# Optimization experiments

Hardware: AMD Instinct MI355X
Metric: run time of the kernel (lower is better)

The kernel has to match this reference:

```python
import jax, jax.numpy as jnp
import numpy as np

B, S, C, DM, NH, DH = 1, 2048, 2048, 768, 12, 64
LN_EPS = 1e-9


def setup_inputs() -> dict:
    rng = jax.random.key(0)
    ks = jax.random.split(rng, 24)
    f32 = jnp.float32
    p = 0.02  # param init scale
    inp = {
        'query': jax.random.normal(ks[0], (B, S, DM), f32),
        'key': jax.random.normal(ks[1], (B, C, DM), f32),
        'value': jax.random.normal(ks[2], (B, C, DM), f32),
        'phi': jax.random.normal(ks[3], (S, DM), f32) * p,
        'pi': jax.random.normal(ks[4], (S, DM), f32) * p,
        'psi': jax.random.normal(ks[5], (C, DM), f32) * p,
        'omega': jax.random.normal(ks[6], (C, DM), f32) * p,
        'cls_mask': jnp.ones((S, C), f32),
        'token_type_mat': jax.random.randint(ks[7], (B, S, C), 0, 2).astype(bool),
        'attention_mask': jnp.ones((B, C), jnp.int32),
        # learned parameters
        'Wq': jax.random.normal(ks[8], (DM, NH * DH), f32) * p,
        'Wk': jax.random.normal(ks[9], (DM, NH * DH), f32) * p,
        'bk': jnp.zeros((NH * DH,), f32),
        'Wv': jax.random.normal(ks[10], (DM, NH * DH), f32) * p,
        'bv': jnp.zeros((NH * DH,), f32),
        'r_w_bias': jax.random.normal(ks[11], (NH, DH), f32) * p,
        'r_r_bias': jax.random.normal(ks[12], (NH, DH), f32) * p,
        'r_kernel': jax.random.normal(ks[13], (DM, NH, DH), f32) * p,
        'r_s_bias': jax.random.normal(ks[14], (NH, DH), f32) * p,
        'seg_embed': jax.random.normal(ks[15], (2, NH, DH), f32) * p,
        'Wo': jax.random.normal(ks[16], (NH * DH, DM), f32) * p,
        'bo': jnp.zeros((DM,), f32),
        'ln_scale': jnp.ones((DM,), f32),
        'ln_bias': jnp.zeros((DM,), f32),
    }
    return inp


def reference(query, key, value, phi, pi, psi, omega, cls_mask,
              token_type_mat, attention_mask,
              Wq, Wk, bk, Wv, bv, r_w_bias, r_r_bias, r_kernel,
              r_s_bias, seg_embed, Wo, bo, ln_scale, ln_bias):
    b, s, _ = query.shape
    c = key.shape[1]
    scale = 1.0 / DH ** 0.5
    # head projections
    q = (query @ Wq).reshape(b, s, NH, DH) * scale          # [b,i,n,h]
    k = (key @ Wk + bk).reshape(b, c, NH, DH)                # [b,j,n,h]
    v = (value @ Wv + bv).reshape(b, c, NH, DH)
    # content score
    content = jnp.einsum('binh,bjnh->bnij', q + r_w_bias * scale, k)
    # factorized relative positional attention
    qr = jnp.einsum('binh,dnh->bind', q + r_r_bias * scale, r_kernel)  # [b,i,n,d_model]
    pos = (jnp.einsum('bind,jd->bnij', qr * phi[:, None], psi)
           + jnp.einsum('bind,jd->bnij', qr * pi[:, None], omega))
    pos = pos * cls_mask
    # token-type attention
    tt_bias = jnp.einsum('binh,snh->bnis', q + r_s_bias * scale, seg_embed)  # [b,n,i,2]
    diff_tt, same_tt = jnp.split(tt_bias, 2, axis=-1)  # each [b,n,i,1]
    tt = jnp.where(token_type_mat[:, None], same_tt, diff_tt) * cls_mask
    # combine, mask, softmax
    score = content + pos + tt
    score = score - 1000000.0 * (1.0 - attention_mask[:, None, None].astype(jnp.float32))
    prob = jax.nn.softmax(score, axis=-1)  # [b,n,i,j]
    attn_vec = jnp.einsum('bnij,bjnh->binh', prob, v).reshape(b, s, NH * DH)
    attn_out = attn_vec @ Wo + bo
    # residual + layernorm
    x = query + attn_out
    mu = x.mean(-1, keepdims=True)
    var = x.var(-1, keepdims=True)
    return (x - mu) * jax.lax.rsqrt(var + LN_EPS) * ln_scale + ln_bias
```

## Files before the change

kernel.cpp:

```cpp
#include <hip/hip_runtime.h>
#include <hip/hip_bf16.h>
#include <stddef.h>

#define DEVINL __device__ __forceinline__

typedef __attribute__((ext_vector_type(8))) short short8;
typedef __attribute__((ext_vector_type(4))) float f32x4;

static constexpr int S_LEN = 2048;
static constexpr int C_LEN = 2048;
static constexpr int DMODEL = 768;
static constexpr int NHEAD = 12;
static constexpr int DHEAD = 64;
static constexpr float SCALE = 0.125f;

DEVINL float bf2f(short s) {
    union { unsigned u; float f; } v;
    v.u = ((unsigned)(unsigned short)s) << 16;
    return v.f;
}
DEVINL short f2bf(float f) {
    union { float f; unsigned u; } v;
    v.f = f;
    unsigned r = v.u + 0x7FFFu + ((v.u >> 16) & 1u);
    return (short)(r >> 16);
}
DEVINL f32x4 zero4() { f32x4 z; z[0]=0.f; z[1]=0.f; z[2]=0.f; z[3]=0.f; return z; }

DEVINL int swz(int width, int row, int col) {
    return (row * width + col) ^ ((row & 7) << 3);
}

DEVINL void gl_lds16(const short* g, short* l) {
    __builtin_amdgcn_global_load_lds(
        (const __attribute__((address_space(1))) void*)g,
        (__attribute__((address_space(3))) void*)l,
        16, 0, 0);
}

template<int ROWS, int WIDTH>
DEVINL void stage_lds_swz(short* lds_tile, const short* src, int src_stride, int w, int lane) {
    constexpr int CPR = WIDTH / 8;
    constexpr int CH  = ROWS * CPR;
    for (int c0 = w * 64; c0 < CH; c0 += 256) {
        int chunk = c0 + lane;
        int row   = chunk / CPR;
        int ccol  = chunk % CPR;
        int scol  = ccol ^ (row & 7);
        gl_lds16(src + (size_t)row * src_stride + scol * 8, lds_tile + c0 * 8);
    }
}

DEVINL void stage_addcol(short* dst, const short* src, const float* p1, const float* p2,
                         int col0, int src_stride) {
    for (int c = threadIdx.x; c < 1024; c += 256) {
        int row = c >> 3;
        int cc  = (c & 7) * 8;
        short8 a = *(const short8*)(src + (size_t)row * src_stride + cc);
        short8 r;
#pragma unroll
        for (int e = 0; e < 8; ++e)
            r[e] = f2bf(bf2f(a[e]) + (p1[col0 + cc + e] - p2[col0 + cc + e]) * SCALE);
        *(short8*)(dst + swz(64, row, cc)) = r;
    }
}

DEVINL void mfma_step_128(const short* As, const short* Bs, f32x4 acc[4][4],
                          int wr, int wc, int lane) {
#pragma unroll
    for (int kk = 0; kk < 64; kk += 32) {
        short8 a[4], b[4];
#pragma unroll
        for (int mi = 0; mi < 4; ++mi)
            a[mi] = *(const short8*)(As + swz(64, wr*64 + mi*16 + (lane & 15), kk + (lane >> 4) * 8));
#pragma unroll
        for (int ni = 0; ni < 4; ++ni)
            b[ni] = *(const short8*)(Bs + swz(64, wc*64 + ni*16 + (lane & 15), kk + (lane >> 4) * 8));
#pragma unroll
        for (int mi = 0; mi < 4; ++mi)
#pragma unroll
            for (int ni = 0; ni < 4; ++ni)
                acc[mi][ni] = __builtin_amdgcn_mfma_f32_16x16x32_bf16(a[mi], b[ni], acc[mi][ni], 0, 0, 0);
    }
}

DEVINL void mfma_2x2(const short* As, const short* Bs, f32x4 acc[2][4],
                     int wr2, int wc2, int lane) {
#pragma unroll
    for (int kk = 0; kk < 64; kk += 32) {
        short8 a[2], b[4];
#pragma unroll
        for (int mi = 0; mi < 2; ++mi)
            a[mi] = *(const short8*)(As + swz(64, wr2*32 + mi*16 + (lane & 15), kk + (lane >> 4) * 8));
#pragma unroll
        for (int nj = 0; nj < 4; ++nj)
            b[nj] = *(const short8*)(Bs + swz(64, wc2*64 + nj*16 + (lane & 15), kk + (lane >> 4) * 8));
#pragma unroll
        for (int mi = 0; mi < 2; ++mi)
#pragma unroll
            for (int nj = 0; nj < 4; ++nj)
                acc[mi][nj] = __builtin_amdgcn_mfma_f32_16x16x32_bf16(a[mi], b[nj], acc[mi][nj], 0, 0, 0);
    }
}

template<int KSTEPS>
DEVINL void gemm128_body(const short* A, const short* Bt, short* As, short* Bs,
                         f32x4 acc[4][4], int wr, int wc, int lane, int w) {
    for (int ks = 0; ks < KSTEPS; ++ks) {
        if (ks) __syncthreads();
        stage_lds_swz<128, 64>(As, A + ks * 64, DMODEL, w, lane);
        stage_lds_swz<128, 64>(Bs, Bt + ks * 64, DMODEL, w, lane);
        __syncthreads();
        mfma_step_128(As, Bs, acc, wr, wc, lane);
    }
}

__global__ void conv_kernel(const float* q, const float* k, const float* v,
                            const float* psi, const float* omega, const float* rk,
                            const float* cls, const int* ttm,
                            short* qc, short* kc, short* vc,
                            short* psc, short* omc, short* rkc,
                            short* clsb, char* ttm8) {
    int z = blockIdx.z;
    if (z == 7) {
        for (int i = blockIdx.x * 256 + threadIdx.x; i < 1048576; i += gridDim.x * 256) {
            int4 t = *(const int4*)(ttm + (size_t)i * 4);
            char4 o;
            o.x = (char)t.x; o.y = (char)t.y; o.z = (char)t.z; o.w = (char)t.w;
            *(char4*)(ttm8 + (size_t)i * 4) = o;
        }
        return;
    }
    const float* src; short* dst; int n4;
    switch (z) {
        case 0: src = q;     dst = qc;   n4 = 393216;  break;
        case 1: src = k;     dst = kc;   n4 = 393216;  break;
        case 2: src = v;     dst = vc;   n4 = 393216;  break;
        case 3: src = psi;   dst = psc;  n4 = 393216;  break;
        case 4: src = omega; dst = omc;  n4 = 393216;  break;
        case 5: src = rk;    dst = rkc;  n4 = 147456;  break;
        default: src = cls;  dst = clsb; n4 = 1048576; break;
    }
    for (int i = blockIdx.x * 256 + threadIdx.x; i < n4; i += gridDim.x * 256) {
        float4 f = *(const float4*)(src + (size_t)i * 4);
        short4 o;
        o.x = f2bf(f.x); o.y = f2bf(f.y); o.z = f2bf(f.z); o.w = f2bf(f.w);
        *(short4*)(dst + (size_t)i * 4) = o;
    }
}

__global__ void transpose_kernel(const float* wq, const float* wk, const float* wv, const float* wo,
                                 short* wqt, short* wkt, short* wvt, short* wot) {
    __shared__ float tile[64][65];
    int z = blockIdx.z;
    const float* src = (z == 0) ? wq : (z == 1) ? wk : (z == 2) ? wv : wo;
    short*       dst = (z == 0) ? wqt : (z == 1) ? wkt : (z == 2) ? wvt : wot;
    int r0 = blockIdx.x * 64, c0 = blockIdx.y * 64;
    for (int e = threadIdx.x; e < 4096; e += 256) {
        int rr = e >> 6, cc = e & 63;
        tile[rr][cc] = src[(size_t)(r0 + rr) * DMODEL + c0 + cc];
    }
    __syncthreads();
    for (int e = threadIdx.x; e < 4096; e += 256) {
        int rr = e >> 6, cc = e & 63;
        dst[(size_t)(c0 + rr) * DMODEL + r0 + cc] = f2bf(tile[cc][rr]);
    }
}

__global__ __launch_bounds__(256, 2)
void qkv_kernel(const short* qc, const short* kc, const short* vc,
                const short* wqt, const short* wkt, const short* wvt,
                const float* bk, const float* bv, const float* rw,
                short* qw_a, short* kpack, short* vt) {
    __shared__ short As[128 * 64], Bs[128 * 64];
    int z = blockIdx.z;
    const short* A  = (z == 0) ? qc  : (z == 1) ? kc  : vc;
    const short* Bt = (z == 0) ? wqt : (z == 1) ? wkt : wvt;
    int i0 = blockIdx.x * 128, c0 = blockIdx.y * 128;
    int t = threadIdx.x, lane = t & 63, w = t >> 6, wr = w >> 1, wc = w & 1;

    f32x4 acc[4][4];
#pragma unroll
    for (int mi = 0; mi < 4; ++mi)
#pragma unroll
        for (int ni = 0; ni < 4; ++ni) acc[mi][ni] = zero4();

    gemm128_body<12>(A + (size_t)i0 * DMODEL, Bt + (size_t)c0 * DMODEL, As, Bs, acc, wr, wc, lane, w);

#pragma unroll
    for (int mi = 0; mi < 4; ++mi)
#pragma unroll
        for (int ni = 0; ni < 4; ++ni)
#pragma unroll
            for (int r = 0; r < 4; ++r) {
                int row = i0 + wr*64 + mi*16 + ((lane >> 4) << 2) + r;
                int col = c0 + wc*64 + ni*16 + (lane & 15);
                float v = acc[mi][ni][r];
                if (z == 0) {
                    qw_a[(size_t)row * DMODEL + col] = f2bf(v * SCALE + rw[col] * SCALE);
                } else if (z == 1) {
                    float vv = v + bk[col];
                    kpack[((size_t)(col >> 6) * C_LEN + row) * DHEAD + (col & 63)] = f2bf(vv);
                } else {
                    float vv = v + bv[col];
                    vt[((size_t)(col >> 6) * DHEAD + (col & 63)) * C_LEN + row] = f2bf(vv);
                }
            }
}

__global__ __launch_bounds__(256, 2)
void qr_kernel(const short* qwa, const short* rkc, const float* rr, const float* rw,
               const float* phi, const float* pi_, short* a1, short* a2, int n_base) {
    __shared__ short As[128 * 64], Bs[128 * 64];
    int nl = blockIdx.z, n = n_base + nl;
    int i0 = blockIdx.x * 128, d0 = blockIdx.y * 128;
    int t = threadIdx.x, lane = t & 63, w = t >> 6, wr = w >> 1, wc = w & 1;

    f32x4 acc[4][4];
#pragma unroll
    for (int mi = 0; mi < 4; ++mi)
#pragma unroll
        for (int ni = 0; ni < 4; ++ni) acc[mi][ni] = zero4();

    stage_addcol(As, qwa + (size_t)i0 * DMODEL + n * DHEAD, rr, rw, n * DHEAD, DMODEL);
    stage_lds_swz<128, 64>(Bs, rkc + (size_t)d0 * DMODEL + n * DHEAD, DMODEL, w, lane);
    __syncthreads();
    mfma_step_128(As, Bs, acc, wr, wc, lane);

#pragma unroll
    for (int mi = 0; mi < 4; ++mi)
#pragma unroll
        for (int ni = 0; ni < 4; ++ni)
#pragma unroll
            for (int r = 0; r < 4; ++r) {
                int row = i0 + wr*64 + mi*16 + ((lane >> 4) << 2) + r;
                int col = d0 + wc*64 + ni*16 + (lane & 15);
                float v = acc[mi][ni][r];
                size_t src = (size_t)row * DMODEL + col;
                size_t dst = ((size_t)nl * S_LEN + row) * DMODEL + col;
                a1[dst] = f2bf(v * phi[src]);
                a2[dst] = f2bf(v * pi_[src]);
            }
}

__global__ void ttb_kernel(const short* qwa, const float* seg, const float* rs, const float* rw,
                           float* ttd, float* tts) {
    int idx = blockIdx.x * 256 + threadIdx.x;
    int n = idx >> 11, i = idx & 2047;
    const short* q  = qwa + (size_t)i * DMODEL + n * DHEAD;
    const float* e0 = seg + n * DHEAD;
    const float* e1 = seg + NHEAD * DHEAD + n * DHEAD;
    float s0 = 0.f, s1 = 0.f;
#pragma unroll
    for (int h = 0; h < DHEAD; ++h) {
        float qv = bf2f(q[h]) + (rs[n * DHEAD + h] - rw[n * DHEAD + h]) * SCALE;
        s0 += qv * e0[h];
        s1 += qv * e1[h];
    }
    ttd[n * S_LEN + i] = s0;
    tts[n * S_LEN + i] = s1;
}

__global__ __launch_bounds__(256, 3)
void flash_kernel(const short* qw_a, const short* kpack, const short* a1, const short* a2,
                  const short* psc, const short* omc, const short* clsb,
                  const char* ttm8, const int* amask, const float* ttd, const float* tts,
                  const short* vt, short* pacc, float* pm, float* pl, int n_base) {
    __shared__ short dbuf[2 * 12288];
    short* Ps = dbuf;

    int nl = blockIdx.y, n = n_base + nl;
    int i0 = blockIdx.x * 64;
    int jt = blockIdx.z;
    int j0 = jt * 128;

    int t = threadIdx.x, lane = t & 63, w = t >> 6;
    int wr2 = w >> 1, wc2 = w & 1;
    int lrow = lane >> 4;
    int lcol = lane & 15;

    f32x4 acc_c[2][4], acc_p[2][4];
#pragma unroll
    for (int mi = 0; mi < 2; ++mi)
#pragma unroll
        for (int nj = 0; nj < 4; ++nj) { acc_c[mi][nj] = zero4(); acc_p[mi][nj] = zero4(); }

    const short* a_base = a1 + ((size_t)nl * S_LEN + i0) * DMODEL;
    const short* a2base = a2 + ((size_t)nl * S_LEN + i0) * DMODEL;
    const short* p_base = psc + (size_t)j0 * DMODEL;
    const short* o_base = omc + (size_t)j0 * DMODEL;

    auto STAGE = [&](int b, int s) {
        short* B = dbuf + b * 12288;
        if (s == 0) {
            stage_lds_swz<64, 64>(B, qw_a + (size_t)i0 * DMODEL + n * DHEAD, DMODEL, w, lane);
            stage_lds_swz<128, 64>(B + 4096, kpack + ((size_t)n * C_LEN + j0) * DHEAD, DHEAD, w, lane);
        } else {
            int d0 = ((s - 1) % 12) * 64;
            const short* asrc = ((s <= 12) ? a_base : a2base) + d0;
            const short* bsrc = ((s <= 12) ? p_base : o_base) + d0;
            stage_lds_swz<64, 64>(B, asrc, DMODEL, w, lane);
            stage_lds_swz<128, 64>(B + 4096, bsrc, DMODEL, w, lane);
        }
    };

    STAGE(0, 0);
    STAGE(1, 1);

    for (int ks = 0; ks < 25; ++ks) {
        int cur = ks & 1;
        short* B = dbuf + cur * 12288;
        if (ks < 24) { asm volatile("s_waitcnt vmcnt(6)" ::: "memory"); }
        else         { asm volatile("s_waitcnt vmcnt(4)" ::: "memory"); }
        __builtin_amdgcn_sched_barrier(0);
        __builtin_amdgcn_s_barrier();
        if (ks == 0) mfma_2x2(B, B + 4096, acc_c, wr2, wc2, lane);
        else         mfma_2x2(B, B + 4096, acc_p, wr2, wc2, lane);
        asm volatile("s_waitcnt lgkmcnt(0)" ::: "memory");
        __builtin_amdgcn_sched_barrier(0);
        __builtin_amdgcn_s_barrier();
        if (ks < 23)
            STAGE(cur, ks + 2);
        else if (ks == 23)
            stage_lds_swz<64, 128>(dbuf + 12288, vt + (size_t)(n * DHEAD) * C_LEN + j0, C_LEN, w, lane);
    }

    float tdiff[2][4], tsame[2][4];
#pragma unroll
    for (int mi = 0; mi < 2; ++mi)
#pragma unroll
        for (int r = 0; r < 4; ++r) {
            int ig = i0 + wr2*32 + mi*16 + lrow*4 + r;
            tdiff[mi][r] = ttd[n * S_LEN + ig];
            tsame[mi][r] = tts[n * S_LEN + ig];
        }
    float pbuf[2][4][4];
    float m[2][4];
#pragma unroll
    for (int mi = 0; mi < 2; ++mi)
#pragma unroll
        for (int r = 0; r < 4; ++r) m[mi][r] = -1.0e9f;
#pragma unroll
    for (int nj = 0; nj < 4; ++nj) {
        int jg = j0 + wc2*64 + nj*16 + lcol;
        float pen = 1.0e6f * (1.0f - (float)amask[jg]);
#pragma unroll
        for (int mi = 0; mi < 2; ++mi)
#pragma unroll
            for (int r = 0; r < 4; ++r) {
                int ig = i0 + wr2*32 + mi*16 + lrow*4 + r;
                size_t eidx = (size_t)ig * C_LEN + jg;
                float clsv = bf2f(clsb[eidx]);
                float ttv  = ttm8[eidx] ? tsame[mi][r] : tdiff[mi][r];
                float sc = acc_c[mi][nj][r] + clsv * (acc_p[mi][nj][r] + ttv) - pen;
                pbuf[mi][nj][r] = sc;
                m[mi][r] = fmaxf(m[mi][r], sc);
            }
    }
#pragma unroll
    for (int mi = 0; mi < 2; ++mi)
#pragma unroll
        for (int r = 0; r < 4; ++r) {
            float v = m[mi][r];
            v = fmaxf(v, __shfl_xor(v, 1));
            v = fmaxf(v, __shfl_xor(v, 2));
            v = fmaxf(v, __shfl_xor(v, 4));
            v = fmaxf(v, __shfl_xor(v, 8));
            m[mi][r] = v;
        }
    float l[2][4];
#pragma unroll
    for (int mi = 0; mi < 2; ++mi)
#pragma unroll
        for (int r = 0; r < 4; ++r) l[mi][r] = 0.f;
#pragma unroll
    for (int nj = 0; nj < 4; ++nj)
#pragma unroll
        for (int mi = 0; mi < 2; ++mi)
#pragma unroll
            for (int r = 0; r < 4; ++r) {
                float pv = __expf(fminf(pbuf[mi][nj][r] - m[mi][r], 0.0f));
                pbuf[mi][nj][r] = pv;
                l[mi][r] += pv;
            }
#pragma unroll
    for (int mi = 0; mi < 2; ++mi)
#pragma unroll
        for (int r = 0; r < 4; ++r) {
            float v = l[mi][r];
            v += __shfl_xor(v, 1);
            v += __shfl_xor(v, 2);
            v += __shfl_xor(v, 4);
            v += __shfl_xor(v, 8);
            l[mi][r] = v;
        }

#pragma unroll
    for (int mi = 0; mi < 2; ++mi)
#pragma unroll
        for (int nj = 0; nj < 4; ++nj)
#pragma unroll
            for (int r = 0; r < 4; ++r)
                Ps[swz(128, wr2*32 + mi*16 + lrow*4 + r, wc2*64 + nj*16 + lcol)] = f2bf(pbuf[mi][nj][r]);

    __syncthreads();

    f32x4 out_acc[2][4];
#pragma unroll
    for (int mi = 0; mi < 2; ++mi)
#pragma unroll
        for (int nh = 0; nh < 4; ++nh) out_acc[mi][nh] = zero4();
#pragma unroll
    for (int kk = 0; kk < 2; ++kk) {
        short8 pa[2];
#pragma unroll
        for (int mi = 0; mi < 2; ++mi)
            pa[mi] = *(const short8*)(Ps + swz(128, wr2*32 + mi*16 + (lane & 15), wc2*64 + kk*32 + lrow*8));
#pragma unroll
        for (int nh = 0; nh < 4; ++nh) {
            short8 vb = *(const short8*)(dbuf + 12288 + swz(128, nh*16 + (lane & 15), wc2*64 + kk*32 + lrow*8));
#pragma unroll
            for (int mi = 0; mi < 2; ++mi)
                out_acc[mi][nh] = __builtin_amdgcn_mfma_f32_16x16x32_bf16(pa[mi], vb, out_acc[mi][nh], 0, 0, 0);
        }
    }

    int jp = jt * 2 + wc2;
#pragma unroll
    for (int mi = 0; mi < 2; ++mi)
#pragma unroll
        for (int r = 0; r < 4; ++r) {
            int ig = i0 + wr2*32 + mi*16 + lrow*4 + r;
            size_t base = ((size_t)(nl * S_LEN + ig) * 32 + jp);
            if (lcol == 0) { pm[base] = m[mi][r]; pl[base] = l[mi][r]; }
#pragma unroll
            for (int nh = 0; nh < 4; ++nh)
                pacc[base * 64 + nh*16 + lcol] = f2bf(out_acc[mi][nh][r]);
        }
}

__global__ void combine_kernel(const short* pacc, const float* pm, const float* pl,
                               short* avec, int n_base) {
    int idx = blockIdx.x * 256 + threadIdx.x;
    int h8 = idx & 7;
    int rest = idx >> 3;
    int i  = rest & 2047;
    int nl = rest >> 11;
    size_t b = ((size_t)nl * S_LEN + i) * 32;
    float M = -1.0e30f;
#pragma unroll
    for (int p = 0; p < 32; ++p) M = fmaxf(M, pm[b + p]);
    float L = 0.f;
    float o[8] = {0.f,0.f,0.f,0.f,0.f,0.f,0.f,0.f};
#pragma unroll
    for (int p = 0; p < 32; ++p) {
        float wg = __expf(pm[b + p] - M);
        L += wg * pl[b + p];
        short8 v = *(const short8*)(pacc + (b + p) * 64 + h8 * 8);
#pragma unroll
        for (int e = 0; e < 8; ++e) o[e] += wg * bf2f(v[e]);
    }
    float invL = 1.0f / L;
    short8 r;
#pragma unroll
    for (int e = 0; e < 8; ++e) r[e] = f2bf(o[e] * invL);
    *(short8*)(avec + (size_t)i * DMODEL + (n_base + nl) * DHEAD + h8 * 8) = r;
}

__global__ __launch_bounds__(256, 2)
void outproj_kernel(const short* avec, const short* wot, const float* bo,
                    const float* query, float* X) {
    __shared__ short As[128 * 64], Bs[128 * 64];
    int i0 = blockIdx.x * 128, c0 = blockIdx.y * 128;
    int t = threadIdx.x, lane = t & 63, w = t >> 6, wr = w >> 1, wc = w & 1;

    f32x4 acc[4][4];
#pragma unroll
    for (int mi = 0; mi < 4; ++mi)
#pragma unroll
        for (int ni = 0; ni < 4; ++ni) acc[mi][ni] = zero4();

    gemm128_body<12>(avec + (size_t)i0 * DMODEL, wot + (size_t)c0 * DMODEL, As, Bs, acc, wr, wc, lane, w);

#pragma unroll
    for (int mi = 0; mi < 4; ++mi)
#pragma unroll
        for (int ni = 0; ni < 4; ++ni)
#pragma unroll
            for (int r = 0; r < 4; ++r) {
                int row = i0 + wr*64 + mi*16 + ((lane >> 4) << 2) + r;
                int col = c0 + wc*64 + ni*16 + (lane & 15);
                float v = acc[mi][ni][r] + bo[col];
                X[(size_t)row * DMODEL + col] = v + query[(size_t)row * DMODEL + col];
            }
}

__global__ void ln_kernel(const float* X, const float* gam, const float* bet, float* out) {
    int row = blockIdx.x, t = threadIdx.x;
    const float* xr = X + (size_t)row * DMODEL;
    float x0 = xr[t], x1 = xr[t + 256], x2 = xr[t + 512];
    float s = x0 + x1 + x2;
    float q = x0*x0 + x1*x1 + x2*x2;
#pragma unroll
    for (int d = 1; d < 64; d <<= 1) { s += __shfl_xor(s, d); q += __shfl_xor(q, d); }
    __shared__ float rs_[4], rq_[4];
    int w = t >> 6, lane = t & 63;
    if (lane == 0) { rs_[w] = s; rq_[w] = q; }
    __syncthreads();
    s = rs_[0] + rs_[1] + rs_[2] + rs_[3];
    q = rq_[0] + rq_[1] + rq_[2] + rq_[3];
    float mu  = s * (1.0f / 768.0f);
    float var = q * (1.0f / 768.0f) - mu * mu;
    float rstd = rsqrtf(fmaxf(var, 0.0f) + 1e-9f);
    out[(size_t)row * DMODEL + t]       = (x0 - mu) * rstd * gam[t]       + bet[t];
    out[(size_t)row * DMODEL + t + 256] = (x1 - mu) * rstd * gam[t + 256] + bet[t + 256];
    out[(size_t)row * DMODEL + t + 512] = (x2 - mu) * rstd * gam[t + 512] + bet[t + 512];
}

extern "C" void kernel_launch(void* const* d_in, const int* in_sizes, int n_in,
                              void* d_out, int out_size, void* d_ws, size_t ws_size,
                              hipStream_t stream) {
    const float* query = (const float*)d_in[0];
    const float* key   = (const float*)d_in[1];
    const float* value = (const float*)d_in[2];
    const float* phi   = (const float*)d_in[3];
    const float* pi_   = (const float*)d_in[4];
    const float* psi   = (const float*)d_in[5];
    const float* omega = (const float*)d_in[6];
    const float* cls   = (const float*)d_in[7];
    const int*   ttm   = (const int*)d_in[8];
    const int*   am    = (const int*)d_in[9];
    const float* Wq    = (const float*)d_in[10];
    const float* Wk    = (const float*)d_in[11];
    const float* bk    = (const float*)d_in[12];
    const float* Wv    = (const float*)d_in[13];
    const float* bv    = (const float*)d_in[14];
    const float* rw    = (const float*)d_in[15];
    const float* rr    = (const float*)d_in[16];
    const float* rk    = (const float*)d_in[17];
    const float* rs    = (const float*)d_in[18];
    const float* seg   = (const float*)d_in[19];
    const float* Wo    = (const float*)d_in[20];
    const float* bo    = (const float*)d_in[21];
    const float* lng   = (const float*)d_in[22];
    const float* lnb   = (const float*)d_in[23];

    char* ws = (char*)d_ws;
    constexpr size_t SZ_W   = 768ull * 768 * 2;
    constexpr size_t SZ_SD  = 2048ull * 768 * 2;
    constexpr size_t SZ_3H  = 3ull * 2048 * 768 * 2;
    constexpr size_t OFF_WQT = 0;
    constexpr size_t OFF_WKT = OFF_WQT + SZ_W;
    constexpr size_t OFF_WVT = OFF_WKT + SZ_W;
    constexpr size_t OFF_WOT = OFF_WVT + SZ_W;
    constexpr size_t OFF_RKC = OFF_WOT + SZ_W;
    constexpr size_t OFF_QC  = OFF_RKC + SZ_W;
    constexpr size_t OFF_KC  = OFF_QC  + SZ_SD;
    constexpr size_t OFF_VC  = OFF_KC  + SZ_SD;
    constexpr size_t OFF_PSC = OFF_VC  + SZ_SD;
    constexpr size_t OFF_OMC = OFF_PSC + SZ_SD;
    constexpr size_t OFF_QWA = OFF_OMC + SZ_SD;
    constexpr size_t OFF_KP  = OFF_QWA + SZ_SD;
    constexpr size_t OFF_VT  = OFF_KP  + SZ_SD;
    constexpr size_t OFF_A1  = OFF_VT  + SZ_SD;
    constexpr size_t OFF_A2  = OFF_A1  + SZ_3H;
    constexpr size_t OFF_CLB = OFF_A2  + SZ_3H;
    constexpr size_t OFF_TT8 = OFF_CLB + 2048ull * 2048 * 2;
    constexpr size_t OFF_TTD = OFF_TT8 + 2048ull * 2048;
    constexpr size_t OFF_TTS = OFF_TTD + 12ull * 2048 * 4;
    constexpr size_t OFF_AV  = OFF_TTS + 12ull * 2048 * 4;
    constexpr size_t OFF_PA  = OFF_AV  + SZ_SD;
    constexpr size_t OFF_PM  = OFF_PA  + 3ull * 2048 * 32 * 64 * 2;
    constexpr size_t OFF_PL  = OFF_PM  + 3ull * 2048 * 32 * 4;
    constexpr size_t OFF_X   = OFF_PA;
    constexpr size_t NEED    = OFF_PL + 3ull * 2048 * 32 * 4;

    if (ws_size < NEED) return;

    short* wqt  = (short*)(ws + OFF_WQT);
    short* wkt  = (short*)(ws + OFF_WKT);
    short* wvt  = (short*)(ws + OFF_WVT);
    short* wot  = (short*)(ws + OFF_WOT);
    short* rkc  = (short*)(ws + OFF_RKC);
    short* qc   = (short*)(ws + OFF_QC);
    short* kc   = (short*)(ws + OFF_KC);
    short* vc   = (short*)(ws + OFF_VC);
    short* psc  = (short*)(ws + OFF_PSC);
    short* omc  = (short*)(ws + OFF_OMC);
    short* qwa  = (short*)(ws + OFF_QWA);
    short* kp   = (short*)(ws + OFF_KP);
    short* vt   = (short*)(ws + OFF_VT);
    short* a1   = (short*)(ws + OFF_A1);
    short* a2   = (short*)(ws + OFF_A2);
    short* clsb = (short*)(ws + OFF_CLB);
    char*  ttm8 = (char*)(ws + OFF_TT8);
    float* ttd  = (float*)(ws + OFF_TTD);
    float* tts  = (float*)(ws + OFF_TTS);
    short* avec = (short*)(ws + OFF_AV);
    short* pacc = (short*)(ws + OFF_PA);
    float* pm   = (float*)(ws + OFF_PM);
    float* pl   = (float*)(ws + OFF_PL);
    float* X    = (float*)(ws + OFF_X);

    conv_kernel<<<dim3(768, 1, 8), 256, 0, stream>>>(query, key, value, psi, omega, rk, cls, ttm,
                                                     qc, kc, vc, psc, omc, rkc, clsb, ttm8);
    transpose_kernel<<<dim3(12, 12, 4), 256, 0, stream>>>(Wq, Wk, Wv, Wo, wqt, wkt, wvt, wot);
    qkv_kernel<<<dim3(16, 6, 3), 256, 0, stream>>>(qc, kc, vc, wqt, wkt, wvt,
                                                   bk, bv, rw, qwa, kp, vt);
    ttb_kernel<<<96, 256, 0, stream>>>(qwa, seg, rs, rw, ttd, tts);
    for (int nb = 0; nb < NHEAD; nb += 3) {
        qr_kernel<<<dim3(16, 6, 3), 256, 0, stream>>>(qwa, rkc, rr, rw, phi, pi_, a1, a2, nb);
        flash_kernel<<<dim3(32, 3, 16), 256, 0, stream>>>(qwa, kp, a1, a2, psc, omc, clsb,
                                                          ttm8, am, ttd, tts, vt, pacc, pm, pl, nb);
        combine_kernel<<<192, 256, 0, stream>>>(pacc, pm, pl, avec, nb);
    }
    outproj_kernel<<<dim3(16, 6), 256, 0, stream>>>(avec, wot, bo, query, X);
    ln_kernel<<<2048, 256, 0, stream>>>(X, lng, lnb, (float*)d_out);
}
```

Baseline: 461.3 us.

## Split flash tile across eight waves instead of four

The flash kernel now launches 512 threads per block. Each of eight waves computes a 16x64 sub-tile instead of a 32x64 one, which halves the per-wave accumulators and MFMA work. LDS staging loops stride by 512 threads and the vmcnt waits are halved to match the fewer loads per thread. This aims to raise latency hiding and wave-level parallelism within the 64x128 tile. In exchange, A-fragment reuse across mi drops and each wave does more LDS traffic per MFMA.

```diff
diff --git a/kernel.cpp b/kernel.cpp
--- a/kernel.cpp
+++ b/kernel.cpp
@@ -38,11 +38,11 @@
         16, 0, 0);
 }
 
-template<int ROWS, int WIDTH>
+template<int ROWS, int WIDTH, int NT = 256>
 DEVINL void stage_lds_swz(short* lds_tile, const short* src, int src_stride, int w, int lane) {
     constexpr int CPR = WIDTH / 8;
     constexpr int CH  = ROWS * CPR;
-    for (int c0 = w * 64; c0 < CH; c0 += 256) {
+    for (int c0 = w * 64; c0 < CH; c0 += NT) {
         int chunk = c0 + lane;
         int row   = chunk / CPR;
         int ccol  = chunk % CPR;
@@ -84,22 +84,18 @@
     }
 }
 
-DEVINL void mfma_2x2(const short* As, const short* Bs, f32x4 acc[2][4],
-                     int wr2, int wc2, int lane) {
+DEVINL void mfma_8w(const short* As, const short* Bs, f32x4 acc[4],
+                    int wr4, int wc, int lane) {
 #pragma unroll
     for (int kk = 0; kk < 64; kk += 32) {
-        short8 a[2], b[4];
-#pragma unroll
-        for (int mi = 0; mi < 2; ++mi)
-            a[mi] = *(const short8*)(As + swz(64, wr2*32 + mi*16 + (lane & 15), kk + (lane >> 4) * 8));
+        short8 a = *(const short8*)(As + swz(64, wr4*16 + (lane & 15), kk + (lane >> 4) * 8));
+        short8 b[4];
 #pragma unroll
         for (int nj = 0; nj < 4; ++nj)
-            b[nj] = *(const short8*)(Bs + swz(64, wc2*64 + nj*16 + (lane & 15), kk + (lane >> 4) * 8));
-#pragma unroll
-        for (int mi = 0; mi < 2; ++mi)
-#pragma unroll
-            for (int nj = 0; nj < 4; ++nj)
-                acc[mi][nj] = __builtin_amdgcn_mfma_f32_16x16x32_bf16(a[mi], b[nj], acc[mi][nj], 0, 0, 0);
+            b[nj] = *(const short8*)(Bs + swz(64, wc*64 + nj*16 + (lane & 15), kk + (lane >> 4) * 8));
+#pragma unroll
+        for (int nj = 0; nj < 4; ++nj)
+            acc[nj] = __builtin_amdgcn_mfma_f32_16x16x32_bf16(a, b[nj], acc[nj], 0, 0, 0);
     }
 }
 
@@ -261,7 +257,7 @@
     tts[n * S_LEN + i] = s1;
 }
 
-__global__ __launch_bounds__(256, 3)
+__global__ __launch_bounds__(512, 2)
 void flash_kernel(const short* qw_a, const short* kpack, const short* a1, const short* a2,
                   const short* psc, const short* omc, const short* clsb,
                   const char* ttm8, const int* amask, const float* ttd, const float* tts,
@@ -275,15 +271,13 @@
     int j0 = jt * 128;
 
     int t = threadIdx.x, lane = t & 63, w = t >> 6;
-    int wr2 = w >> 1, wc2 = w & 1;
+    int wr4 = w >> 1, wc = w & 1;
     int lrow = lane >> 4;
     int lcol = lane & 15;
 
-    f32x4 acc_c[2][4], acc_p[2][4];
-#pragma unroll
-    for (int mi = 0; mi < 2; ++mi)
-#pragma unroll
-        for (int nj = 0; nj < 4; ++nj) { acc_c[mi][nj] = zero4(); acc_p[mi][nj] = zero4(); }
+    f32x4 acc_c[4], acc_p[4];
+#pragma unroll
+    for (int nj = 0; nj < 4; ++nj) { acc_c[nj] = zero4(); acc_p[nj] = zero4(); }
 
     const short* a_base = a1 + ((size_t)nl * S_LEN + i0) * DMODEL;
     const short* a2base = a2 + ((size_t)nl * S_LEN + i0) * DMODEL;
@@ -293,14 +287,14 @@
     auto STAGE = [&](int b, int s) {
         short* B = dbuf + b * 12288;
         if (s == 0) {
-            stage_lds_swz<64, 64>(B, qw_a + (size_t)i0 * DMODEL + n * DHEAD, DMODEL, w, lane);
-            stage_lds_swz<128, 64>(B + 4096, kpack + ((size_t)n * C_LEN + j0) * DHEAD, DHEAD, w, lane);
+            stage_lds_swz<64, 64, 512>(B, qw_a + (size_t)i0 * DMODEL + n * DHEAD, DMODEL, w, lane);
+            stage_lds_swz<128, 64, 512>(B + 4096, kpack + ((size_t)n * C_LEN + j0) * DHEAD, DHEAD, w, lane);
         } else {
             int d0 = ((s - 1) % 12) * 64;
             const short* asrc = ((s <= 12) ? a_base : a2base) + d0;
             const short* bsrc = ((s <= 12) ? p_base : o_base) + d0;
-            stage_lds_swz<64, 64>(B, asrc, DMODEL, w, lane);
-            stage_lds_swz<128, 64>(B + 4096, bsrc, DMODEL, w, lane);
+            stage_lds_swz<64, 64, 512>(B, asrc, DMODEL, w, lane);
+            stage_lds_swz<128, 64, 512>(B + 4096, bsrc, DMODEL, w, lane);
         }
     };
 
@@ -310,133 +304,104 @@
     for (int ks = 0; ks < 25; ++ks) {
         int cur = ks & 1;
         short* B = dbuf + cur * 12288;
-        if (ks < 24) { asm volatile("s_waitcnt vmcnt(6)" ::: "memory"); }
-        else         { asm volatile("s_waitcnt vmcnt(4)" ::: "memory"); }
+        if (ks < 24) { asm volatile("s_waitcnt vmcnt(3)" ::: "memory"); }
+        else         { asm volatile("s_waitcnt vmcnt(2)" ::: "memory"); }
         __builtin_amdgcn_sched_barrier(0);
         __builtin_amdgcn_s_barrier();
-        if (ks == 0) mfma_2x2(B, B + 4096, acc_c, wr2, wc2, lane);
-        else         mfma_2x2(B, B + 4096, acc_p, wr2, wc2, lane);
+        mfma_8w(B, B + 4096, (ks == 0) ? acc_c : acc_p, wr4, wc, lane);
         asm volatile("s_waitcnt lgkmcnt(0)" ::: "memory");
         __builtin_amdgcn_sched_barrier(0);
         __builtin_amdgcn_s_barrier();
         if (ks < 23)
             STAGE(cur, ks + 2);
         else if (ks == 23)
-            stage_lds_swz<64, 128>(dbuf + 12288, vt + (size_t)(n * DHEAD) * C_LEN + j0, C_LEN, w, lane);
-    }
-
-    float tdiff[2][4], tsame[2][4];
-#pragma unroll
-    for (int mi = 0; mi < 2; ++mi)
+            stage_lds_swz<64, 128, 512>(dbuf + 12288, vt + (size_t)(n * DHEAD) * C_LEN + j0, C_LEN, w, lane);
+    }
+
+    float tdiff[4], tsame[4];
+#pragma unroll
+    for (int r = 0; r < 4; ++r) {
+        int ig = i0 + wr4*16 + lrow*4 + r;
+        tdiff[r] = ttd[n * S_LEN + ig];
+        tsame[r] = tts[n * S_LEN + ig];
+    }
+    float pbuf[4][4];
+    float m[4] = { -1.0e9f, -1.0e9f, -1.0e9f, -1.0e9f };
+#pragma unroll
+    for (int nj = 0; nj < 4; ++nj) {
+        int jg = j0 + wc*64 + nj*16 + lcol;
+        float pen = 1.0e6f * (1.0f - (float)amask[jg]);
 #pragma unroll
         for (int r = 0; r < 4; ++r) {
-            int ig = i0 + wr2*32 + mi*16 + lrow*4 + r;
-            tdiff[mi][r] = ttd[n * S_LEN + ig];
-            tsame[mi][r] = tts[n * S_LEN + ig];
+            int ig = i0 + wr4*16 + lrow*4 + r;
+            size_t eidx = (size_t)ig * C_LEN + jg;
+            float clsv = bf2f(clsb[eidx]);
+            float ttv  = ttm8[eidx] ? tsame[r] : tdiff[r];
+            float sc = acc_c[nj][r] + clsv * (acc_p[nj][r] + ttv) - pen;
+            pbuf[nj][r] = sc;
+            m[r] = fmaxf(m[r], sc);
         }
-    float pbuf[2][4][4];
-    float m[2][4];
-#pragma unroll
-    for (int mi = 0; mi < 2; ++mi)
-#pragma unroll
-        for (int r = 0; r < 4; ++r) m[mi][r] = -1.0e9f;
-#pragma unroll
-    for (int nj = 0; nj < 4; ++nj) {
-        int jg = j0 + wc2*64 + nj*16 + lcol;
-        float pen = 1.0e6f * (1.0f - (float)amask[jg]);
-#pragma unroll
-        for (int mi = 0; mi < 2; ++mi)
-#pragma unroll
-            for (int r = 0; r < 4; ++r) {
-                int ig = i0 + wr2*32 + mi*16 + lrow*4 + r;
-                size_t eidx = (size_t)ig * C_LEN + jg;
-                float clsv = bf2f(clsb[eidx]);
-                float ttv  = ttm8[eidx] ? tsame[mi][r] : tdiff[mi][r];
-                float sc = acc_c[mi][nj][r] + clsv * (acc_p[mi][nj][r] + ttv) - pen;
-                pbuf[mi][nj][r] = sc;
-                m[mi][r] = fmaxf(m[mi][r], sc);
-            }
-    }
-#pragma unroll
-    for (int mi = 0; mi < 2; ++mi)
+    }
+#pragma unroll
+    for (int r = 0; r < 4; ++r) {
+        float v = m[r];
+        v = fmaxf(v, __shfl_xor(v, 1));
+        v = fmaxf(v, __shfl_xor(v, 2));
+        v = fmaxf(v, __shfl_xor(v, 4));
+        v = fmaxf(v, __shfl_xor(v, 8));
+        m[r] = v;
+    }
+    float l[4] = { 0.f, 0.f, 0.f, 0.f };
+#pragma unroll
+    for (int nj = 0; nj < 4; ++nj)
 #pragma unroll
         for (int r = 0; r < 4; ++r) {
-            float v = m[mi][r];
-            v = fmaxf(v, __shfl_xor(v, 1));
-            v = fmaxf(v, __shfl_xor(v, 2));
-            v = fmaxf(v, __shfl_xor(v, 4));
-            v = fmaxf(v, __shfl_xor(v, 8));
-            m[mi][r] = v;
+            float pv = __expf(fminf(pbuf[nj][r] - m[r], 0.0f));
+            pbuf[nj][r] = pv;
+            l[r] += pv;
         }
-    float l[2][4];
-#pragma unroll
-    for (int mi = 0; mi < 2; ++mi)
-#pragma unroll
-        for (int r = 0; r < 4; ++r) l[mi][r] = 0.f;
+#pragma unroll
+    for (int r = 0; r < 4; ++r) {
+        float v = l[r];
+        v += __shfl_xor(v, 1);
+        v += __shfl_xor(v, 2);
+        v += __shfl_xor(v, 4);
+        v += __shfl_xor(v, 8);
+        l[r] = v;
+    }
+
 #pragma unroll
     for (int nj = 0; nj < 4; ++nj)
 #pragma unroll
-        for (int mi = 0; mi < 2; ++mi)
-#pragma unroll
-            for (int r = 0; r < 4; ++r) {
-                float pv = __expf(fminf(pbuf[mi][nj][r] - m[mi][r], 0.0f));
-                pbuf[mi][nj][r] = pv;
-                l[mi][r] += pv;
-            }
-#pragma unroll
-    for (int mi = 0; mi < 2; ++mi)
-#pragma unroll
-        for (int r = 0; r < 4; ++r) {
-            float v = l[mi][r];
-            v += __shfl_xor(v, 1);
-            v += __shfl_xor(v, 2);
-            v += __shfl_xor(v, 4);
-            v += __shfl_xor(v, 8);
-            l[mi][r] = v;
+        for (int r = 0; r < 4; ++r)
+            Ps[swz(128, wr4*16 + lrow*4 + r, wc*64 + nj*16 + lcol)] = f2bf(pbuf[nj][r]);
+
+    __syncthreads();
+
+    const short* Vlds = dbuf + 12288;
+    f32x4 out_acc[4];
+#pragma unroll
+    for (int nh = 0; nh < 4; ++nh) out_acc[nh] = zero4();
+#pragma unroll
+    for (int kk = 0; kk < 2; ++kk) {
+        short8 pa = *(const short8*)(Ps + swz(128, wr4*16 + (lane & 15), wc*64 + kk*32 + lrow*8));
+#pragma unroll
+        for (int nh = 0; nh < 4; ++nh) {
+            short8 vb = *(const short8*)(Vlds + swz(128, nh*16 + (lane & 15), wc*64 + kk*32 + lrow*8));
+            out_acc[nh] = __builtin_amdgcn_mfma_f32_16x16x32_bf16(pa, vb, out_acc[nh], 0, 0, 0);
         }
-
-#pragma unroll
-    for (int mi = 0; mi < 2; ++mi)
-#pragma unroll
-        for (int nj = 0; nj < 4; ++nj)
-#pragma unroll
-            for (int r = 0; r < 4; ++r)
-                Ps[swz(128, wr2*32 + mi*16 + lrow*4 + r, wc2*64 + nj*16 + lcol)] = f2bf(pbuf[mi][nj][r]);
-
-    __syncthreads();
-
-    f32x4 out_acc[2][4];
-#pragma unroll
-    for (int mi = 0; mi < 2; ++mi)
-#pragma unroll
-        for (int nh = 0; nh < 4; ++nh) out_acc[mi][nh] = zero4();
-#pragma unroll
-    for (int kk = 0; kk < 2; ++kk) {
-        short8 pa[2];
-#pragma unroll
-        for (int mi = 0; mi < 2; ++mi)
-            pa[mi] = *(const short8*)(Ps + swz(128, wr2*32 + mi*16 + (lane & 15), wc2*64 + kk*32 + lrow*8));
-#pragma unroll
-        for (int nh = 0; nh < 4; ++nh) {
-            short8 vb = *(const short8*)(dbuf + 12288 + swz(128, nh*16 + (lane & 15), wc2*64 + kk*32 + lrow*8));
-#pragma unroll
-            for (int mi = 0; mi < 2; ++mi)
-                out_acc[mi][nh] = __builtin_amdgcn_mfma_f32_16x16x32_bf16(pa[mi], vb, out_acc[mi][nh], 0, 0, 0);
-        }
-    }
-
-    int jp = jt * 2 + wc2;
-#pragma unroll
-    for (int mi = 0; mi < 2; ++mi)
-#pragma unroll
-        for (int r = 0; r < 4; ++r) {
-            int ig = i0 + wr2*32 + mi*16 + lrow*4 + r;
-            size_t base = ((size_t)(nl * S_LEN + ig) * 32 + jp);
-            if (lcol == 0) { pm[base] = m[mi][r]; pl[base] = l[mi][r]; }
-#pragma unroll
-            for (int nh = 0; nh < 4; ++nh)
-                pacc[base * 64 + nh*16 + lcol] = f2bf(out_acc[mi][nh][r]);
-        }
+    }
+
+    int jp = jt * 2 + wc;
+#pragma unroll
+    for (int r = 0; r < 4; ++r) {
+        int ig = i0 + wr4*16 + lrow*4 + r;
+        size_t base = ((size_t)(nl * S_LEN + ig) * 32 + jp);
+        if (lcol == 0) { pm[base] = m[r]; pl[base] = l[r]; }
+#pragma unroll
+        for (int nh = 0; nh < 4; ++nh)
+            pacc[base * 64 + nh*16 + lcol] = f2bf(out_acc[nh][r]);
+    }
 }
 
 __global__ void combine_kernel(const short* pacc, const float* pm, const float* pl,
@@ -610,7 +575,7 @@
     ttb_kernel<<<96, 256, 0, stream>>>(qwa, seg, rs, rw, ttd, tts);
     for (int nb = 0; nb < NHEAD; nb += 3) {
         qr_kernel<<<dim3(16, 6, 3), 256, 0, stream>>>(qwa, rkc, rr, rw, phi, pi_, a1, a2, nb);
-        flash_kernel<<<dim3(32, 3, 16), 256, 0, stream>>>(qwa, kp, a1, a2, psc, omc, clsb,
+        flash_kernel<<<dim3(32, 3, 16), 512, 0, stream>>>(qwa, kp, a1, a2, psc, omc, clsb,
                                                           ttm8, am, ttd, tts, vt, pacc, pm, pl, nb);
         combine_kernel<<<192, 256, 0, stream>>>(pacc, pm, pl, avec, nb);
     }
```

Measured after the change: 525.5 us. +13.9%, slower.

## Triple-buffer flash kernel LDS staging and drop per-iteration second barrier

Applied to the files above, without the earlier changes.

The flash kernel's K-loop moves from double to triple buffering in LDS. The next-next stage is now issued before the MFMA work on the current buffer, so the second workgroup barrier in each iteration can be removed and loads overlap compute. The P tile gets its own third buffer. The cost is that LDS per block grows by half and launch bounds drop from 3 to 2 blocks per CU, which lowers occupancy. The workspace layout is regrouped under a chunk constant, with the same values as before.

```diff
diff --git a/kernel.cpp b/kernel.cpp
--- a/kernel.cpp
+++ b/kernel.cpp
@@ -261,13 +261,13 @@
     tts[n * S_LEN + i] = s1;
 }
 
-__global__ __launch_bounds__(256, 3)
+__global__ __launch_bounds__(256, 2)
 void flash_kernel(const short* qw_a, const short* kpack, const short* a1, const short* a2,
                   const short* psc, const short* omc, const short* clsb,
                   const char* ttm8, const int* amask, const float* ttd, const float* tts,
                   const short* vt, short* pacc, float* pm, float* pl, int n_base) {
-    __shared__ short dbuf[2 * 12288];
-    short* Ps = dbuf;
+    __shared__ short dbuf[3 * 12288];
+    short* Ps = dbuf + 2 * 12288;
 
     int nl = blockIdx.y, n = n_base + nl;
     int i0 = blockIdx.x * 64;
@@ -308,21 +308,18 @@
     STAGE(1, 1);
 
     for (int ks = 0; ks < 25; ++ks) {
-        int cur = ks & 1;
-        short* B = dbuf + cur * 12288;
+        short* B = dbuf + (ks % 3) * 12288;
         if (ks < 24) { asm volatile("s_waitcnt vmcnt(6)" ::: "memory"); }
         else         { asm volatile("s_waitcnt vmcnt(4)" ::: "memory"); }
         __builtin_amdgcn_sched_barrier(0);
         __builtin_amdgcn_s_barrier();
-        if (ks == 0) mfma_2x2(B, B + 4096, acc_c, wr2, wc2, lane);
-        else         mfma_2x2(B, B + 4096, acc_p, wr2, wc2, lane);
+        if (ks < 23)
+            STAGE((ks + 2) % 3, ks + 2);
+        else if (ks == 23)
+            stage_lds_swz<64, 128>(dbuf + 12288, vt + (size_t)(n * DHEAD) * C_LEN + j0, C_LEN, w, lane);
+        mfma_2x2(B, B + 4096, (ks == 0) ? acc_c : acc_p, wr2, wc2, lane);
         asm volatile("s_waitcnt lgkmcnt(0)" ::: "memory");
         __builtin_amdgcn_sched_barrier(0);
-        __builtin_amdgcn_s_barrier();
-        if (ks < 23)
-            STAGE(cur, ks + 2);
-        else if (ks == 23)
-            stage_lds_swz<64, 128>(dbuf + 12288, vt + (size_t)(n * DHEAD) * C_LEN + j0, C_LEN, w, lane);
     }
 
     float tdiff[2][4], tsame[2][4];
@@ -405,6 +402,7 @@
 
     __syncthreads();
 
+    const short* Vlds = dbuf + 12288;
     f32x4 out_acc[2][4];
 #pragma unroll
     for (int mi = 0; mi < 2; ++mi)
@@ -418,7 +416,7 @@
             pa[mi] = *(const short8*)(Ps + swz(128, wr2*32 + mi*16 + (lane & 15), wc2*64 + kk*32 + lrow*8));
 #pragma unroll
         for (int nh = 0; nh < 4; ++nh) {
-            short8 vb = *(const short8*)(dbuf + 12288 + swz(128, nh*16 + (lane & 15), wc2*64 + kk*32 + lrow*8));
+            short8 vb = *(const short8*)(Vlds + swz(128, nh*16 + (lane & 15), wc2*64 + kk*32 + lrow*8));
 #pragma unroll
             for (int mi = 0; mi < 2; ++mi)
                 out_acc[mi][nh] = __builtin_amdgcn_mfma_f32_16x16x32_bf16(pa[mi], vb, out_acc[mi][nh], 0, 0, 0);
@@ -548,7 +546,6 @@
     char* ws = (char*)d_ws;
     constexpr size_t SZ_W   = 768ull * 768 * 2;
     constexpr size_t SZ_SD  = 2048ull * 768 * 2;
-    constexpr size_t SZ_3H  = 3ull * 2048 * 768 * 2;
     constexpr size_t OFF_WQT = 0;
     constexpr size_t OFF_WKT = OFF_WQT + SZ_W;
     constexpr size_t OFF_WVT = OFF_WKT + SZ_W;
@@ -562,18 +559,23 @@
     constexpr size_t OFF_QWA = OFF_OMC + SZ_SD;
     constexpr size_t OFF_KP  = OFF_QWA + SZ_SD;
     constexpr size_t OFF_VT  = OFF_KP  + SZ_SD;
-    constexpr size_t OFF_A1  = OFF_VT  + SZ_SD;
-    constexpr size_t OFF_A2  = OFF_A1  + SZ_3H;
-    constexpr size_t OFF_CLB = OFF_A2  + SZ_3H;
+    constexpr size_t OFF_CLB = OFF_VT  + SZ_SD;
     constexpr size_t OFF_TT8 = OFF_CLB + 2048ull * 2048 * 2;
     constexpr size_t OFF_TTD = OFF_TT8 + 2048ull * 2048;
     constexpr size_t OFF_TTS = OFF_TTD + 12ull * 2048 * 4;
     constexpr size_t OFF_AV  = OFF_TTS + 12ull * 2048 * 4;
-    constexpr size_t OFF_PA  = OFF_AV  + SZ_SD;
-    constexpr size_t OFF_PM  = OFF_PA  + 3ull * 2048 * 32 * 64 * 2;
-    constexpr size_t OFF_PL  = OFF_PM  + 3ull * 2048 * 32 * 4;
-    constexpr size_t OFF_X   = OFF_PA;
-    constexpr size_t NEED    = OFF_PL + 3ull * 2048 * 32 * 4;
+    constexpr size_t FIX_END = OFF_AV + SZ_SD;
+
+    constexpr size_t CH = 3;
+    constexpr size_t SZ_A  = CH * 2048ull * 768 * 2;
+    constexpr size_t OFF_A1 = FIX_END;
+    constexpr size_t OFF_A2 = OFF_A1 + SZ_A;
+    constexpr size_t OFF_PA = OFF_A2 + SZ_A;
+    constexpr size_t SZ_PA = CH * 2048ull * 32 * 64 * 2;
+    constexpr size_t OFF_PM = OFF_PA + SZ_PA;
+    constexpr size_t SZ_PM = CH * 2048ull * 32 * 4;
+    constexpr size_t OFF_PL = OFF_PM + SZ_PM;
+    constexpr size_t NEED   = OFF_PL + SZ_PM;
 
     if (ws_size < NEED) return;
 
@@ -590,17 +592,17 @@
     short* qwa  = (short*)(ws + OFF_QWA);
     short* kp   = (short*)(ws + OFF_KP);
     short* vt   = (short*)(ws + OFF_VT);
-    short* a1   = (short*)(ws + OFF_A1);
-    short* a2   = (short*)(ws + OFF_A2);
     short* clsb = (short*)(ws + OFF_CLB);
     char*  ttm8 = (char*)(ws + OFF_TT8);
     float* ttd  = (float*)(ws + OFF_TTD);
     float* tts  = (float*)(ws + OFF_TTS);
     short* avec = (short*)(ws + OFF_AV);
+    short* a1   = (short*)(ws + OFF_A1);
+    short* a2   = (short*)(ws + OFF_A2);
     short* pacc = (short*)(ws + OFF_PA);
     float* pm   = (float*)(ws + OFF_PM);
     float* pl   = (float*)(ws + OFF_PL);
-    float* X    = (float*)(ws + OFF_X);
+    float* X    = (float*)(ws + OFF_PA);
 
     conv_kernel<<<dim3(768, 1, 8), 256, 0, stream>>>(query, key, value, psi, omega, rk, cls, ttm,
                                                      qc, kc, vc, psc, omc, rkc, clsb, ttm8);
@@ -608,11 +610,11 @@
     qkv_kernel<<<dim3(16, 6, 3), 256, 0, stream>>>(qc, kc, vc, wqt, wkt, wvt,
                                                    bk, bv, rw, qwa, kp, vt);
     ttb_kernel<<<96, 256, 0, stream>>>(qwa, seg, rs, rw, ttd, tts);
-    for (int nb = 0; nb < NHEAD; nb += 3) {
-        qr_kernel<<<dim3(16, 6, 3), 256, 0, stream>>>(qwa, rkc, rr, rw, phi, pi_, a1, a2, nb);
-        flash_kernel<<<dim3(32, 3, 16), 256, 0, stream>>>(qwa, kp, a1, a2, psc, omc, clsb,
-                                                          ttm8, am, ttd, tts, vt, pacc, pm, pl, nb);
-        combine_kernel<<<192, 256, 0, stream>>>(pacc, pm, pl, avec, nb);
+    for (int nb = 0; nb < NHEAD; nb += CH) {
+        qr_kernel<<<dim3(16, 6, CH), 256, 0, stream>>>(qwa, rkc, rr, rw, phi, pi_, a1, a2, nb);
+        flash_kernel<<<dim3(32, CH, 16), 256, 0, stream>>>(qwa, kp, a1, a2, psc, omc, clsb,
+                                                           ttm8, am, ttd, tts, vt, pacc, pm, pl, nb);
+        combine_kernel<<<CH * 64, 256, 0, stream>>>(pacc, pm, pl, avec, nb);
     }
     outproj_kernel<<<dim3(16, 6), 256, 0, stream>>>(avec, wot, bo, query, X);
     ln_kernel<<<2048, 256, 0, stream>>>(X, lng, lnb, (float*)d_out);
```

New measurement: 655.8 us. 42.2% more time.
